# Kernel tuning notes

Hardware: AMD Instinct MI355X
Metric: run time of the kernel (lower is better)

## Reference

```python
import jax, jax.numpy as jnp
import numpy as np

DT = 0.001
TAU_M = 0.02
TAU_S = 0.005
ALPHA = 1.0 - DT / TAU_S  # synaptic decay = 0.8
BETA = 1.0 - DT / TAU_M   # membrane decay = 0.95


def setup_inputs() -> dict:
    key = jax.random.key(0)
    k1, k2 = jax.random.split(key)
    steps, batch, d1, d2 = 100, 256, 784, 512
    x = (jax.random.uniform(k1, (steps, batch, d1)) < 0.05).astype(jnp.float32)
    # kaiming_normal_ on (d2, d1): std = sqrt(2 / fan_in)
    weight = jax.random.normal(k2, (d2, d1), dtype=jnp.float32) * np.float32(np.sqrt(2.0 / d1))
    return {"x": x, "weight": weight}


def reference(x, weight):
    # x: [steps, batch, d1] spikes; weight: [d2, d1]
    batch = x.shape[1]
    d2 = weight.shape[0]
    zeros = jnp.zeros((batch, d2), dtype=x.dtype)

    def step(carry, x_t):
        I_prev, V_prev = carry
        I = ALPHA * I_prev + x_t @ weight.T            # synaptic current
        V_pre = BETA * V_prev + (1.0 - BETA) * I        # membrane before reset
        s = (V_pre > 1.0).astype(x.dtype)               # threshold crossing
        V = (1.0 - s) * V_pre                           # reset to zero on spike
        return (I, V), s

    # torch loop runs i = 1..steps-1 using input[i-1]; output[0] stays zero
    _, spikes = jax.lax.scan(step, (zeros, zeros), x[:-1])
    return jnp.concatenate([zeros[None], spikes], axis=0)  # [steps, batch, d2]
```

## Files before the change

kernel.cpp:

```cpp
#include <hip/hip_runtime.h>

#define STEPS 100
#define BATCH 256
#define D1 784
#define D1P 785
#define D2 512
#define NSTEP 99
#define NTB (NSTEP * BATCH)
#define LIST_PAD 80

#define JS 32
#define G32_LDS (D1P * JS * 4)
#define NCHUNK 16
#define CHUNK_TB (NTB / NCHUNK)

#define L1_LISTS_OFF 0
#define L1_LISTS_BYTES ((size_t)NTB * LIST_PAD * 2)
#define L1_CNTS_OFF  L1_LISTS_BYTES
#define L1_CNTS_BYTES ((size_t)NTB * 4)
#define L1_Z_OFF     (((L1_CNTS_OFF + L1_CNTS_BYTES) + 255) & ~(size_t)255)
#define Z_BYTES      ((size_t)NTB * D2 * 4)
#define WS_T1        (L1_Z_OFF + Z_BYTES)

#define WT_BYTES  (D1P * D2 * 4)
#define T2_Z_OFF  ((size_t)((WT_BYTES + 255) & ~255))
#define WS_T2     (T2_Z_OFF + Z_BYTES)

#define HALF1 392
#define HCAP  64


__global__ __launch_bounds__(256) void prep_lists(
    const float* __restrict__ x, unsigned short* __restrict__ lists,
    unsigned int* __restrict__ cnt16s)
{
    const int wid  = blockIdx.x * 4 + (threadIdx.x >> 6);
    const int lane = threadIdx.x & 63;
    const float* xt = x + (size_t)wid * D1;
    unsigned short* lp = lists + (size_t)wid * LIST_PAD;
    const unsigned long long lt = (1ull << lane) - 1ull;

    int cnt = 0;
    for (int base = 0; base < D1; base += 256) {
        const int i0 = base + lane * 4;
        float4 v = make_float4(0.f, 0.f, 0.f, 0.f);
        if (i0 < D1) v = *(const float4*)(xt + i0);
        const bool a0 = v.x > 0.5f, a1 = v.y > 0.5f;
        const bool a2 = v.z > 0.5f, a3 = v.w > 0.5f;
        const unsigned long long m0 = __ballot(a0);
        const unsigned long long m1 = __ballot(a1);
        const unsigned long long m2 = __ballot(a2);
        const unsigned long long m3 = __ballot(a3);
        int p = cnt + __popcll(m0 & lt) + __popcll(m1 & lt)
                    + __popcll(m2 & lt) + __popcll(m3 & lt);
        if (a0) { if (p < LIST_PAD) lp[p] = (unsigned short)((i0 + 0) << 3); ++p; }
        if (a1) { if (p < LIST_PAD) lp[p] = (unsigned short)((i0 + 1) << 3); ++p; }
        if (a2) { if (p < LIST_PAD) lp[p] = (unsigned short)((i0 + 2) << 3); ++p; }
        if (a3) { if (p < LIST_PAD) lp[p] = (unsigned short)((i0 + 3) << 3); ++p; }
        cnt += __popcll(m0) + __popcll(m1) + __popcll(m2) + __popcll(m3);
    }
    if (cnt > LIST_PAD) cnt = LIST_PAD;
    int cnt16 = (cnt + 15) & ~15;
    if (cnt16 < 16) cnt16 = 16;
    if (lane < cnt16 - cnt) lp[cnt + lane] = (unsigned short)(D1 << 3);
    if (lane == 0) cnt16s[wid] = (unsigned int)cnt16;
}

#define READS8(d0,d1,d2,d3,d4,d5,d6,d7,e)                                      \
    d0 = *(const float4*)(base + (((e.x & 0xFFFFu) << 4) + qd16));             \
    d1 = *(const float4*)(base + (((e.x >> 16)     << 4) + qd16));             \
    d2 = *(const float4*)(base + (((e.y & 0xFFFFu) << 4) + qd16));             \
    d3 = *(const float4*)(base + (((e.y >> 16)     << 4) + qd16));             \
    d4 = *(const float4*)(base + (((e.z & 0xFFFFu) << 4) + qd16));             \
    d5 = *(const float4*)(base + (((e.z >> 16)     << 4) + qd16));             \
    d6 = *(const float4*)(base + (((e.w & 0xFFFFu) << 4) + qd16));             \
    d7 = *(const float4*)(base + (((e.w >> 16)     << 4) + qd16));

#define ACC8(p0,p1,p2,p3,p4,p5,p6,p7)                                          \
    ax += p0.x; ay += p0.y; az += p0.z; aw += p0.w;                            \
    bx += p1.x; by += p1.y; bz += p1.z; bw += p1.w;                            \
    ax += p2.x; ay += p2.y; az += p2.z; aw += p2.w;                            \
    bx += p3.x; by += p3.y; bz += p3.z; bw += p3.w;                            \
    ax += p4.x; ay += p4.y; az += p4.z; aw += p4.w;                            \
    bx += p5.x; by += p5.y; bz += p5.z; bw += p5.w;                            \
    ax += p6.x; ay += p6.y; az += p6.z; aw += p6.w;                            \
    bx += p7.x; by += p7.y; bz += p7.z; bw += p7.w;

__global__ __launch_bounds__(1024, 4) void gather32(
    const float* __restrict__ W,
    const unsigned short* __restrict__ lists,
    const unsigned int* __restrict__ cnt16s,
    float* __restrict__ z)
{
    const int slice = blockIdx.x & 15;
    const int chunk = blockIdx.x >> 4;
    const int j0 = slice * JS;

    extern __shared__ float wt[];

    {
        const int jj = threadIdx.x & 31;
        const int ih = threadIdx.x >> 5;
        const float* wrow = W + (size_t)(j0 + jj) * D1;
        for (int i4 = ih; i4 < 196; i4 += 32) {
            int i = i4 * 4;
            float4 v = *(const float4*)(wrow + i);
            wt[(i + 0) * JS + jj] = v.x;
            wt[(i + 1) * JS + jj] = v.y;
            wt[(i + 2) * JS + jj] = v.z;
            wt[(i + 3) * JS + jj] = v.w;
        }
        if (threadIdx.x < JS) wt[D1 * JS + threadIdx.x] = 0.f;
    }
    __syncthreads();

    const int lane = threadIdx.x & 63;
    const int wv   = threadIdx.x >> 6;
    const int grp  = lane >> 3;
    const unsigned qd16 = (unsigned)((lane & 7) << 4);
    const char* base = (const char*)wt;

    const int tb_end = (chunk + 1) * CHUNK_TB;
    for (int tb = chunk * CHUNK_TB + wv * 8 + grp; tb < tb_end; tb += 128) {
        const unsigned short* lp = lists + (size_t)tb * LIST_PAD;
        const int c16 = (int)cnt16s[tb];
        uint4 rA = *(const uint4*)lp;
        uint4 rB = *(const uint4*)(lp + 8);
        float4 A0, A1, A2, A3, A4, A5, A6, A7;
        float4 B0, B1, B2, B3, B4, B5, B6, B7;
        READS8(A0, A1, A2, A3, A4, A5, A6, A7, rA);
        READS8(B0, B1, B2, B3, B4, B5, B6, B7, rB);
        float ax = 0.f, ay = 0.f, az = 0.f, aw = 0.f;
        float bx = 0.f, by = 0.f, bz = 0.f, bw = 0.f;
        for (int k = 16; k < c16; k += 16) {
            uint4 eA = *(const uint4*)(lp + k);
            uint4 eB = *(const uint4*)(lp + k + 8);
            ACC8(A0, A1, A2, A3, A4, A5, A6, A7)
            READS8(A0, A1, A2, A3, A4, A5, A6, A7, eA);
            ACC8(B0, B1, B2, B3, B4, B5, B6, B7)
            READS8(B0, B1, B2, B3, B4, B5, B6, B7, eB);
        }
        ACC8(A0, A1, A2, A3, A4, A5, A6, A7)
        ACC8(B0, B1, B2, B3, B4, B5, B6, B7)
        float4 r4;
        r4.x = ax + bx; r4.y = ay + by; r4.z = az + bz; r4.w = aw + bw;
        *(float4*)(z + (size_t)tb * D2 + j0 + (int)(qd16 >> 2)) = r4;
    }
}

__global__ __launch_bounds__(256) void lif_scan(
    const float* __restrict__ z, float* __restrict__ out)
{
    const int gid = blockIdx.x * 256 + threadIdx.x;
    out[gid] = 0.f;
    float I = 0.f, V = 0.f;
    const size_t S = (size_t)BATCH * D2;
    const float* zp = z + gid;
    float* op = out + S + gid;
    float zz[16];
    #pragma unroll
    for (int u = 0; u < 16; ++u) zz[u] = zp[(size_t)u * S];
    for (int t0 = 0; t0 < NSTEP; t0 += 16) {
        float zn[16];
        const int tn = t0 + 16;
        #pragma unroll
        for (int u = 0; u < 16; ++u) {
            zn[u] = 0.f;
            if (tn + u < NSTEP) zn[u] = zp[(size_t)(tn + u) * S];
        }
        const int n = (NSTEP - t0 < 16) ? (NSTEP - t0) : 16;
        #pragma unroll
        for (int u = 0; u < 16; ++u)
            if (u < n) {
                I = 0.8f * I + zz[u];
                float Vp = 0.95f * V + 0.05f * I;
                float s = (Vp > 1.0f) ? 1.0f : 0.f;
                V = (1.0f - s) * Vp;
                op[(size_t)(t0 + u) * S] = s;
            }
        #pragma unroll
        for (int u = 0; u < 16; ++u) zz[u] = zn[u];
    }
}

__global__ void transpose_w(const float* __restrict__ W, float* __restrict__ Wt) {
    __shared__ float tile[32][33];
    int i0 = blockIdx.x * 32;
    int j0 = blockIdx.y * 32;
    int tx = threadIdx.x, ty = threadIdx.y;
    for (int r = 0; r < 32; r += 8) {
        int jj = j0 + ty + r, ii = i0 + tx;
        float v = 0.f;
        if (jj < D2 && ii < D1) v = W[jj * D1 + ii];
        tile[ty + r][tx] = v;
    }
    __syncthreads();
    for (int r = 0; r < 32; r += 8) {
        int ii = i0 + ty + r, jj = j0 + tx;
        if (ii < D1P && jj < D2) Wt[ii * D2 + jj] = tile[tx][ty + r];
    }
}

__global__ __launch_bounds__(512) void gather_z(
    const float* __restrict__ x, const float* __restrict__ Wt,
    float* __restrict__ z)
{
    const int g    = threadIdx.x >> 7;
    const int t128 = threadIdx.x & 127;
    const int half = (threadIdx.x >> 6) & 1;
    const int lane = threadIdx.x & 63;
    const int tb   = blockIdx.x * 4 + g;
    __shared__ __align__(16) unsigned int s_off[4][2][HCAP];
    __shared__ int s_cnt[4][2];
    {
        const float* xh = x + (size_t)tb * D1 + half * HALF1;
        unsigned int* lp = s_off[g][half];
        int cnt = 0;
        for (int base = 0; base < HALF1; base += 64) {
            int i = base + lane;
            bool a = (i < HALF1) && (xh[i] > 0.5f);
            unsigned long long m = __ballot(a);
            int pre = __popcll(m & ((1ull << lane) - 1ull));
            if (a) {
                int p = cnt + pre;
                if (p < HCAP) lp[p] = (unsigned int)((half * HALF1 + i) << 11);
            }
            cnt += __popcll(m);
        }
        if (cnt > HCAP) cnt = HCAP;
        int cnt4 = (cnt + 3) & ~3;
        if (lane < cnt4 - cnt) lp[cnt + lane] = (unsigned int)(D1 << 11);
        if (lane == 0) s_cnt[g][half] = cnt4;
    }
    __syncthreads();
    const char* wj = (const char*)Wt + (t128 << 4);
    float ax0 = 0.f, ay0 = 0.f, az0 = 0.f, aw0 = 0.f;
    float ax1 = 0.f, ay1 = 0.f, az1 = 0.f, aw1 = 0.f;
    #pragma unroll
    for (int h = 0; h < 2; ++h) {
        const unsigned int* l = s_off[g][h];
        const int c4 = s_cnt[g][h];
        for (int k = 0; k < c4; k += 4) {
            uint4 o = *(const uint4*)(l + k);
            float4 w0 = *(const float4*)(wj + o.x);
            float4 w1 = *(const float4*)(wj + o.y);
            float4 w2 = *(const float4*)(wj + o.z);
            float4 w3 = *(const float4*)(wj + o.w);
            ax0 += w0.x; ay0 += w0.y; az0 += w0.z; aw0 += w0.w;
            ax1 += w1.x; ay1 += w1.y; az1 += w1.z; aw1 += w1.w;
            ax0 += w2.x; ay0 += w2.y; az0 += w2.z; aw0 += w2.w;
            ax1 += w3.x; ay1 += w3.y; az1 += w3.z; aw1 += w3.w;
        }
    }
    float4 r;
    r.x = ax0 + ax1; r.y = ay0 + ay1; r.z = az0 + az1; r.w = aw0 + aw1;
    *(float4*)(z + (size_t)tb * D2 + (t128 << 2)) = r;
}

__global__ __launch_bounds__(256) void snn_fallback(
    const float* __restrict__ x, const float* __restrict__ Wfull,
    float* __restrict__ out)
{
    const int b = blockIdx.x >> 1;
    const int jhalf = blockIdx.x & 1;
    const int j = jhalf * 256 + threadIdx.x;
    const int lane = threadIdx.x & 63;
    __shared__ int s_cnt;
    __shared__ int s_list[D1];
    out[(size_t)b * D2 + j] = 0.f;
    float I = 0.f, V = 0.f;
    const float* wrow = Wfull + (size_t)j * D1;
    for (int t = 0; t < STEPS - 1; ++t) {
        if (threadIdx.x == 0) s_cnt = 0;
        __syncthreads();
        const float* xt = x + (size_t)(t * BATCH + b) * D1;
        for (int base = 0; base < D1; base += 256) {
            int i = base + threadIdx.x;
            bool active = (i < D1) && (xt[i] > 0.5f);
            unsigned long long mask = __ballot(active);
            int nact = __popcll(mask);
            int pre = __popcll(mask & ((1ull << lane) - 1ull));
            int wb = 0;
            if (lane == 0 && nact) wb = atomicAdd(&s_cnt, nact);
            wb = __shfl(wb, 0);
            if (active) s_list[wb + pre] = i;
        }
        __syncthreads();
        const int cnt = s_cnt;
        float a0 = 0.f, a1 = 0.f, a2 = 0.f, a3 = 0.f;
        int k = 0;
        for (; k + 4 <= cnt; k += 4) {
            a0 += wrow[s_list[k]];     a1 += wrow[s_list[k + 1]];
            a2 += wrow[s_list[k + 2]]; a3 += wrow[s_list[k + 3]];
        }
        for (; k < cnt; ++k) a0 += wrow[s_list[k]];
        float acc = (a0 + a1) + (a2 + a3);
        I = 0.8f * I + acc;
        float Vp = 0.95f * V + 0.05f * I;
        float s = (Vp > 1.0f) ? 1.0f : 0.f;
        V = (1.0f - s) * Vp;
        out[(size_t)(t + 1) * (BATCH * D2) + (size_t)b * D2 + j] = s;
        __syncthreads();
    }
}

extern "C" void kernel_launch(void* const* d_in, const int* in_sizes, int n_in,
                              void* d_out, int out_size, void* d_ws, size_t ws_size,
                              hipStream_t stream) {
    const float* x = (const float*)d_in[0];
    const float* w = (const float*)d_in[1];
    float* out = (float*)d_out;
    char* ws = (char*)d_ws;

    if (ws_size >= WS_T1) {
        static bool g32_init = false;
        if (!g32_init) {
            (void)hipFuncSetAttribute((const void*)gather32,
                hipFuncAttributeMaxDynamicSharedMemorySize, G32_LDS);
            g32_init = true;
        }
        unsigned short* lists = (unsigned short*)(ws + L1_LISTS_OFF);
        unsigned int* cnt16s = (unsigned int*)(ws + L1_CNTS_OFF);
        float* z = (float*)(ws + L1_Z_OFF);
        prep_lists<<<NTB / 4, 256, 0, stream>>>(x, lists, cnt16s);
        gather32<<<256, 1024, G32_LDS, stream>>>(w, lists, cnt16s, z);
        lif_scan<<<BATCH * D2 / 256, 256, 0, stream>>>(z, out);
    } else if (ws_size >= WS_T2) {
        float* wt = (float*)ws;
        float* z  = (float*)(ws + T2_Z_OFF);
        dim3 tg(25, 16), tb(32, 8);
        transpose_w<<<tg, tb, 0, stream>>>(w, wt);
        gather_z<<<NTB / 4, 512, 0, stream>>>(x, wt, z);
        lif_scan<<<BATCH * D2 / 256, 256, 0, stream>>>(z, out);
    } else {
        snn_fallback<<<BATCH * 2, 256, 0, stream>>>(x, w, out);
    }
}
```

Baseline: 186.4 us.

## Fuse sparse gather with LIF scan in LDS and swizzle weight tile

Merges the gather kernel and the LIF scan into one kernel. Each block now owns a 16-batch by 32-neuron tile, computes 8 timesteps of currents per window into a double-buffered LDS area, and the first 512 threads run the LIF recurrence directly from that buffer. This removes the full z tensor's round trip through global memory and one kernel launch. The weight tile in LDS gets an XOR swizzle to reduce bank conflicts, and spike lists for the next window are prefetched. In exchange there is a block-wide barrier per window, half the threads sit idle during the serial scan, and parallelism is bounded to 256 blocks.

```diff
diff --git a/kernel.cpp b/kernel.cpp
--- a/kernel.cpp
+++ b/kernel.cpp
@@ -10,20 +10,19 @@
 #define LIST_PAD 80
 
 #define JS 32
-#define G32_LDS (D1P * JS * 4)
-#define NCHUNK 16
-#define CHUNK_TB (NTB / NCHUNK)
+#define ZBW (D1P * JS)
+#define FUSED_LDS ((ZBW + 2 * 8 * 16 * JS) * 4)
+#define NWIN 13
 
 #define L1_LISTS_OFF 0
 #define L1_LISTS_BYTES ((size_t)NTB * LIST_PAD * 2)
 #define L1_CNTS_OFF  L1_LISTS_BYTES
 #define L1_CNTS_BYTES ((size_t)NTB * 4)
-#define L1_Z_OFF     (((L1_CNTS_OFF + L1_CNTS_BYTES) + 255) & ~(size_t)255)
-#define Z_BYTES      ((size_t)NTB * D2 * 4)
-#define WS_T1        (L1_Z_OFF + Z_BYTES)
+#define WS_T1        (L1_CNTS_OFF + L1_CNTS_BYTES)
 
 #define WT_BYTES  (D1P * D2 * 4)
 #define T2_Z_OFF  ((size_t)((WT_BYTES + 255) & ~255))
+#define Z_BYTES   ((size_t)NTB * D2 * 4)
 #define WS_T2     (T2_Z_OFF + Z_BYTES)
 
 #define HALF1 392
@@ -66,15 +65,14 @@
     if (lane == 0) cnt16s[wid] = (unsigned int)cnt16;
 }
 
+#define RD16(t) (*(const float4*)(base + ((((unsigned)(t)) << 4) + \
+                 (qd16 ^ ((((unsigned)(t)) << 1) & 0x70u)))))
+
 #define READS8(d0,d1,d2,d3,d4,d5,d6,d7,e)                                      \
-    d0 = *(const float4*)(base + (((e.x & 0xFFFFu) << 4) + qd16));             \
-    d1 = *(const float4*)(base + (((e.x >> 16)     << 4) + qd16));             \
-    d2 = *(const float4*)(base + (((e.y & 0xFFFFu) << 4) + qd16));             \
-    d3 = *(const float4*)(base + (((e.y >> 16)     << 4) + qd16));             \
-    d4 = *(const float4*)(base + (((e.z & 0xFFFFu) << 4) + qd16));             \
-    d5 = *(const float4*)(base + (((e.z >> 16)     << 4) + qd16));             \
-    d6 = *(const float4*)(base + (((e.w & 0xFFFFu) << 4) + qd16));             \
-    d7 = *(const float4*)(base + (((e.w >> 16)     << 4) + qd16));
+    d0 = RD16(e.x & 0xFFFFu);  d1 = RD16(e.x >> 16);                           \
+    d2 = RD16(e.y & 0xFFFFu);  d3 = RD16(e.y >> 16);                           \
+    d4 = RD16(e.z & 0xFFFFu);  d5 = RD16(e.z >> 16);                           \
+    d6 = RD16(e.w & 0xFFFFu);  d7 = RD16(e.w >> 16);
 
 #define ACC8(p0,p1,p2,p3,p4,p5,p6,p7)                                          \
     ax += p0.x; ay += p0.y; az += p0.z; aw += p0.w;                            \
@@ -86,65 +84,108 @@
     ax += p6.x; ay += p6.y; az += p6.z; aw += p6.w;                            \
     bx += p7.x; by += p7.y; bz += p7.z; bw += p7.w;
 
-__global__ __launch_bounds__(1024, 4) void gather32(
+__global__ __launch_bounds__(1024, 4) void gather_lif(
     const float* __restrict__ W,
     const unsigned short* __restrict__ lists,
     const unsigned int* __restrict__ cnt16s,
-    float* __restrict__ z)
-{
-    const int slice = blockIdx.x & 15;
-    const int chunk = blockIdx.x >> 4;
+    float* __restrict__ out)
+{
+    const int slice  = blockIdx.x & 15;
+    const int bchunk = blockIdx.x >> 4;
     const int j0 = slice * JS;
+    const int b0 = bchunk * 16;
 
     extern __shared__ float wt[];
 
     {
         const int jj = threadIdx.x & 31;
+        const int q4 = jj & 28;
+        const int c  = jj & 3;
         const int ih = threadIdx.x >> 5;
         const float* wrow = W + (size_t)(j0 + jj) * D1;
         for (int i4 = ih; i4 < 196; i4 += 32) {
             int i = i4 * 4;
             float4 v = *(const float4*)(wrow + i);
-            wt[(i + 0) * JS + jj] = v.x;
-            wt[(i + 1) * JS + jj] = v.y;
-            wt[(i + 2) * JS + jj] = v.z;
-            wt[(i + 3) * JS + jj] = v.w;
+            wt[(i + 0) * JS + ((q4 ^ (((i + 0) & 7) << 2)) | c)] = v.x;
+            wt[(i + 1) * JS + ((q4 ^ (((i + 1) & 7) << 2)) | c)] = v.y;
+            wt[(i + 2) * JS + ((q4 ^ (((i + 2) & 7) << 2)) | c)] = v.z;
+            wt[(i + 3) * JS + ((q4 ^ (((i + 3) & 7) << 2)) | c)] = v.w;
         }
         if (threadIdx.x < JS) wt[D1 * JS + threadIdx.x] = 0.f;
     }
-    __syncthreads();
 
     const int lane = threadIdx.x & 63;
     const int wv   = threadIdx.x >> 6;
+    const int toff = wv >> 1;
     const int grp  = lane >> 3;
+    const int bi   = ((wv & 1) << 3) | grp;
+    const int myb  = b0 + bi;
     const unsigned qd16 = (unsigned)((lane & 7) << 4);
     const char* base = (const char*)wt;
 
-    const int tb_end = (chunk + 1) * CHUNK_TB;
-    for (int tb = chunk * CHUNK_TB + wv * 8 + grp; tb < tb_end; tb += 128) {
-        const unsigned short* lp = lists + (size_t)tb * LIST_PAD;
-        const int c16 = (int)cnt16s[tb];
-        uint4 rA = *(const uint4*)lp;
-        uint4 rB = *(const uint4*)(lp + 8);
-        float4 A0, A1, A2, A3, A4, A5, A6, A7;
-        float4 B0, B1, B2, B3, B4, B5, B6, B7;
-        READS8(A0, A1, A2, A3, A4, A5, A6, A7, rA);
-        READS8(B0, B1, B2, B3, B4, B5, B6, B7, rB);
-        float ax = 0.f, ay = 0.f, az = 0.f, aw = 0.f;
-        float bx = 0.f, by = 0.f, bz = 0.f, bw = 0.f;
-        for (int k = 16; k < c16; k += 16) {
-            uint4 eA = *(const uint4*)(lp + k);
-            uint4 eB = *(const uint4*)(lp + k + 8);
+    float I = 0.f, V = 0.f;
+    size_t obase = 0;
+    if (threadIdx.x < 512) {
+        obase = (size_t)(b0 + (threadIdx.x >> 5)) * D2 + j0 + (threadIdx.x & 31);
+        out[obase] = 0.f;
+    }
+
+    int tb0 = toff * BATCH + myb;
+    uint4 cE0 = *(const uint4*)(lists + (size_t)tb0 * LIST_PAD);
+    uint4 cE1 = *(const uint4*)(lists + (size_t)tb0 * LIST_PAD + 8);
+    int   cC  = (int)cnt16s[tb0];
+
+    __syncthreads();
+
+    for (int w = 0; w < NWIN; ++w) {
+        int tn = (w + 1) * 8 + toff;
+        if (tn > NSTEP - 1) tn = NSTEP - 1;
+        const size_t tbn = (size_t)tn * BATCH + myb;
+        uint4 nE0 = *(const uint4*)(lists + tbn * LIST_PAD);
+        uint4 nE1 = *(const uint4*)(lists + tbn * LIST_PAD + 8);
+        int   nC  = (int)cnt16s[tbn];
+
+        const int t = w * 8 + toff;
+        if (t < NSTEP) {
+            const unsigned short* lp =
+                lists + (size_t)((size_t)t * BATCH + myb) * LIST_PAD;
+            const int c16 = cC;
+            float4 A0, A1, A2, A3, A4, A5, A6, A7;
+            float4 B0, B1, B2, B3, B4, B5, B6, B7;
+            READS8(A0, A1, A2, A3, A4, A5, A6, A7, cE0);
+            READS8(B0, B1, B2, B3, B4, B5, B6, B7, cE1);
+            float ax = 0.f, ay = 0.f, az = 0.f, aw = 0.f;
+            float bx = 0.f, by = 0.f, bz = 0.f, bw = 0.f;
+            for (int k = 16; k < c16; k += 16) {
+                uint4 eA = *(const uint4*)(lp + k);
+                uint4 eB = *(const uint4*)(lp + k + 8);
+                ACC8(A0, A1, A2, A3, A4, A5, A6, A7)
+                READS8(A0, A1, A2, A3, A4, A5, A6, A7, eA);
+                ACC8(B0, B1, B2, B3, B4, B5, B6, B7)
+                READS8(B0, B1, B2, B3, B4, B5, B6, B7, eB);
+            }
             ACC8(A0, A1, A2, A3, A4, A5, A6, A7)
-            READS8(A0, A1, A2, A3, A4, A5, A6, A7, eA);
             ACC8(B0, B1, B2, B3, B4, B5, B6, B7)
-            READS8(B0, B1, B2, B3, B4, B5, B6, B7, eB);
-        }
-        ACC8(A0, A1, A2, A3, A4, A5, A6, A7)
-        ACC8(B0, B1, B2, B3, B4, B5, B6, B7)
-        float4 r4;
-        r4.x = ax + bx; r4.y = ay + by; r4.z = az + bz; r4.w = aw + bw;
-        *(float4*)(z + (size_t)tb * D2 + j0 + (int)(qd16 >> 2)) = r4;
+            float4 r4;
+            r4.x = ax + bx; r4.y = ay + by; r4.z = az + bz; r4.w = aw + bw;
+            *(float4*)(wt + ZBW + (((w & 1) * 8 + toff) * 512)
+                       + bi * JS + ((lane & 7) << 2)) = r4;
+        }
+        __syncthreads();
+        if (threadIdx.x < 512) {
+            const int nt = (w == NWIN - 1) ? 3 : 8;
+            const float* zb = wt + ZBW + (w & 1) * 4096 + threadIdx.x;
+            float* op = out + (size_t)(w * 8 + 1) * (BATCH * D2) + obase;
+            for (int u = 0; u < nt; ++u) {
+                float zv = zb[(size_t)u * 512];
+                I = 0.8f * I + zv;
+                float Vp = 0.95f * V + 0.05f * I;
+                float s = (Vp > 1.0f) ? 1.0f : 0.f;
+                V = (1.0f - s) * Vp;
+                op[(size_t)u * (BATCH * D2)] = s;
+            }
+        }
+        cE0 = nE0; cE1 = nE1; cC = nC;
     }
 }
 
@@ -313,18 +354,16 @@
     char* ws = (char*)d_ws;
 
     if (ws_size >= WS_T1) {
-        static bool g32_init = false;
-        if (!g32_init) {
-            (void)hipFuncSetAttribute((const void*)gather32,
-                hipFuncAttributeMaxDynamicSharedMemorySize, G32_LDS);
-            g32_init = true;
+        static bool gl_init = false;
+        if (!gl_init) {
+            (void)hipFuncSetAttribute((const void*)gather_lif,
+                hipFuncAttributeMaxDynamicSharedMemorySize, FUSED_LDS);
+            gl_init = true;
         }
         unsigned short* lists = (unsigned short*)(ws + L1_LISTS_OFF);
         unsigned int* cnt16s = (unsigned int*)(ws + L1_CNTS_OFF);
-        float* z = (float*)(ws + L1_Z_OFF);
         prep_lists<<<NTB / 4, 256, 0, stream>>>(x, lists, cnt16s);
-        gather32<<<256, 1024, G32_LDS, stream>>>(w, lists, cnt16s, z);
-        lif_scan<<<BATCH * D2 / 256, 256, 0, stream>>>(z, out);
+        gather_lif<<<256, 1024, FUSED_LDS, stream>>>(w, lists, cnt16s, out);
     } else if (ws_size >= WS_T2) {
         float* wt = (float*)ws;
         float* z  = (float*)(ws + T2_Z_OFF);
```

After: 185.2 us. About the same (-0.6%).
